# Performance work log

Measured on AMD Instinct MI355X. Metric: run time of the kernel, lower is better.

The kernel has to match this reference:

```python
import jax, jax.numpy as jnp
import numpy as np

B, C, H, W = 16, 768, 32, 32
HEADS = 12
EPS = 1e-5


def _make_rel_index(h, w):
    coords = np.stack(np.meshgrid(np.arange(h), np.arange(w), indexing='ij'))  # [2,h,w]
    cf = coords.reshape(2, -1)                      # [2,N]
    rel = cf[:, :, None] - cf[:, None, :]           # [2,N,N]
    rel = rel.transpose(1, 2, 0).copy()             # [N,N,2]
    rel[:, :, 0] += h - 1
    rel[:, :, 1] += w - 1
    rel[:, :, 0] *= 2 * w - 1
    return jnp.asarray(rel.sum(-1), dtype=jnp.int32)  # [N,N]


def setup_inputs() -> dict:
    key = jax.random.key(0)
    ks = jax.random.split(key, 8)
    s = 0.02
    return {
        'x': jax.random.normal(ks[0], (B, C, H, W), jnp.float32),
        'rpb_table': jax.random.normal(ks[1], ((2 * H - 1) * (2 * W - 1), HEADS), jnp.float32) * s,
        'g1': jnp.ones((C,), jnp.float32),
        'b1': jnp.zeros((C,), jnp.float32),
        'q_w': jax.random.normal(ks[2], (C, C), jnp.float32) * s,
        'q_b': jnp.zeros((C,), jnp.float32),
        'kv_w': jax.random.normal(ks[3], (2 * C, C), jnp.float32) * s,
        'kv_b': jnp.zeros((2 * C,), jnp.float32),
        'proj_w': jax.random.normal(ks[4], (C, C), jnp.float32) * s,
        'proj_b': jnp.zeros((C,), jnp.float32),
        'g2': jnp.ones((C,), jnp.float32),
        'b2': jnp.zeros((C,), jnp.float32),
        'fc1_w': jax.random.normal(ks[5], (4 * C, C), jnp.float32) * s,
        'fc1_b': jnp.zeros((4 * C,), jnp.float32),
        'fc2_w': jax.random.normal(ks[6], (C, 4 * C), jnp.float32) * s,
        'fc2_b': jnp.zeros((C,), jnp.float32),
        'rel_index': _make_rel_index(H, W),
    }


def _ln(t, g, b):
    m = t.mean(-1, keepdims=True)
    v = ((t - m) ** 2).mean(-1, keepdims=True)
    return (t - m) * jax.lax.rsqrt(v + EPS) * g + b


def reference(x, rpb_table, g1, b1, q_w, q_b, kv_w, kv_b, proj_w, proj_b,
              g2, b2, fc1_w, fc1_b, fc2_w, fc2_b, rel_index):
    b, c, h, w = x.shape
    n = h * w
    heads = rpb_table.shape[1]
    hd = c // heads
    scale = hd ** -0.5

    xt = x.reshape(b, c, n).transpose(0, 2, 1)  # [B,N,C]

    # --- attention branch ---
    xn = _ln(xt, g1, b1)
    q = (xn @ q_w.T + q_b).reshape(b, n, heads, hd).transpose(0, 2, 1, 3)  # [B,h,N,d]
    kv = (xn @ kv_w.T + kv_b).reshape(b, n, 2, heads, hd)
    k = kv[:, :, 0].transpose(0, 2, 1, 3)  # [B,h,N,d]
    v = kv[:, :, 1].transpose(0, 2, 1, 3)  # [B,h,N,d]
    attn = jnp.einsum('bhnd,bhmd->bhnm', q, k) * scale  # [B,h,N,N]
    bias = rpb_table[rel_index].transpose(2, 0, 1)      # [h,N,N]
    attn = jax.nn.softmax(attn + bias[None], axis=-1)
    o = jnp.einsum('bhnm,bhmd->bhnd', attn, v).transpose(0, 2, 1, 3).reshape(b, n, c)
    o = o @ proj_w.T + proj_b
    xt = xt + o

    # --- mlp branch ---
    xn = _ln(xt, g2, b2)
    h1 = jax.nn.gelu(xn @ fc1_w.T + fc1_b, approximate=False)
    xt = xt + (h1 @ fc2_w.T + fc2_b)

    return xt.transpose(0, 2, 1).reshape(b, c, h, w)
```

## Files before the change

### kernel.cpp

```cpp
#include <hip/hip_runtime.h>
#include <hip/hip_bf16.h>
#include <math.h>

typedef unsigned short u16;
typedef unsigned int u32;
typedef float f32x4 __attribute__((ext_vector_type(4)));
typedef short bf16x8 __attribute__((ext_vector_type(8)));
typedef unsigned short us4 __attribute__((ext_vector_type(4)));

struct alignas(16) F4 { float v[4]; };

static constexpr int Bb = 16;
static constexpr int Cc = 768;
static constexpr int Nn = 1024;
static constexpr int NH = 12;
static constexpr int HD = 64;
static constexpr float LOG2E = 1.4426950408889634f;

static __device__ __forceinline__ u16 f2bf(float f) {
  union { float f; unsigned u; } v; v.f = f;
  unsigned u = v.u;
  u += 0x7fffu + ((u >> 16) & 1u);
  return (u16)(u >> 16);
}
static __device__ __forceinline__ float bf2f(u16 x) {
  union { unsigned u; float f; } v; v.u = ((unsigned)x) << 16; return v.f;
}
static __device__ __forceinline__ void gload16(const u16* g, u16* l) {
  __builtin_amdgcn_global_load_lds((const __attribute__((address_space(1))) u32*)g,
                                   (__attribute__((address_space(3))) u32*)l, 16, 0, 0);
}

__global__ __launch_bounds__(256) void k_prep(const float* __restrict__ q_w,
    const float* __restrict__ kv_w, const float* __restrict__ proj_w,
    const float* __restrict__ fc1_w, const float* __restrict__ fc2_w,
    const float* __restrict__ q_b, const float* __restrict__ kv_b,
    u16* __restrict__ wqkv, u16* __restrict__ wproj, u16* __restrict__ wfc1,
    u16* __restrict__ wfc2, float* __restrict__ bqkv) {
  int i = blockIdx.x * 256 + threadIdx.x;
  if (i < 589824)            wqkv[i] = f2bf(q_w[i]);
  else if (i < 1769472)      wqkv[i] = f2bf(kv_w[i - 589824]);
  else if (i < 2359296)      wproj[i - 1769472] = f2bf(proj_w[i - 1769472]);
  else if (i < 4718592)      wfc1[i - 2359296] = f2bf(fc1_w[i - 2359296]);
  else if (i < 7077888)      wfc2[i - 4718592] = f2bf(fc2_w[i - 4718592]);
  else if (i < 7078656)      bqkv[i - 7077888] = q_b[i - 7077888];
  else                       bqkv[i - 7077888] = kv_b[i - 7078656];
}

__global__ void k_transpose(const float* __restrict__ x, float* __restrict__ xt) {
  __shared__ float tile[32][33];
  int b = blockIdx.z, c0 = blockIdx.y * 32, n0 = blockIdx.x * 32;
  int tx = threadIdx.x, ty = threadIdx.y;
  const float* xp = x + (size_t)b * Cc * Nn;
  #pragma unroll
  for (int i = 0; i < 32; i += 8)
    tile[ty + i][tx] = xp[(size_t)(c0 + ty + i) * Nn + n0 + tx];
  __syncthreads();
  float* xtp = xt + (size_t)b * Nn * Cc;
  #pragma unroll
  for (int i = 0; i < 32; i += 8)
    xtp[(size_t)(n0 + ty + i) * Cc + c0 + tx] = tile[tx][ty + i];
}

__global__ __launch_bounds__(256) void k_layernorm(const float* __restrict__ in,
    const float* __restrict__ gam, const float* __restrict__ bet,
    u16* __restrict__ out) {
  int wave = threadIdx.x >> 6, lane = threadIdx.x & 63;
  int row = blockIdx.x * 4 + wave;
  const float* p = in + (size_t)row * Cc;
  float v[12]; float s = 0.f;
  #pragma unroll
  for (int i = 0; i < 12; i++) { v[i] = p[lane + i * 64]; s += v[i]; }
  #pragma unroll
  for (int m = 32; m >= 1; m >>= 1) s += __shfl_xor(s, m);
  float mean = s * (1.f / 768.f);
  float q = 0.f;
  #pragma unroll
  for (int i = 0; i < 12; i++) { float d = v[i] - mean; q += d * d; }
  #pragma unroll
  for (int m = 32; m >= 1; m >>= 1) q += __shfl_xor(q, m);
  float rstd = rsqrtf(q * (1.f / 768.f) + 1e-5f);
  u16* o = out + (size_t)row * Cc;
  #pragma unroll
  for (int i = 0; i < 12; i++) {
    int j = lane + i * 64;
    o[j] = f2bf((v[i] - mean) * rstd * gam[j] + bet[j]);
  }
}

__global__ void k_bias_pre(const float* __restrict__ rpb, const int* __restrict__ rel,
                           u16* __restrict__ out) {
  int idx = blockIdx.x * 256 + threadIdx.x;
  int k = idx & 1023, q = (idx >> 10) & 1023, h = idx >> 20;
  float v = rpb[rel[(size_t)q * Nn + k] * NH + h];
  out[((size_t)h * Nn + q) * Nn + k] = f2bf(v * LOG2E);
}

struct GemmArgs {
  const u16* A; const u16* W; const float* bias;
  int M, N, K;
  const float* resIn;
  float* outF;
  u16* outBf;
  u16 *q, *k, *v;
};

template <int EPI>
__global__ __launch_bounds__(256) void k_gemm(GemmArgs p) {
  __shared__ __align__(16) u16 lA[128 * 32];
  __shared__ __align__(16) u16 lB[128 * 32];
  const int tid = threadIdx.x;
  const int wave = tid >> 6, lane = tid & 63;
  const int l15 = lane & 15, g = lane >> 4;
  const int wrow = wave >> 1, wcol = wave & 1;
  const int nwg = gridDim.x * gridDim.y;
  const int wg = blockIdx.y * gridDim.x + blockIdx.x;
  const int swz = (wg & 7) * (nwg >> 3) + (wg >> 3);
  const int bn = (swz % gridDim.x) * 128, bm = (swz / gridDim.x) * 128;
  const int K = p.K;
  f32x4 acc[4][4];
  #pragma unroll
  for (int i = 0; i < 4; i++)
    #pragma unroll
    for (int j = 0; j < 4; j++) acc[i][j] = (f32x4){0.f, 0.f, 0.f, 0.f};

  const u16* Ab = p.A + (size_t)bm * K;
  const u16* Wb = p.W + (size_t)bn * K;
  const int c0 = tid, c1 = tid + 256;
  const int r0 = c0 >> 2, k80 = (c0 & 3) * 8;
  const int r1 = c1 >> 2, k81 = (c1 & 3) * 8;

  for (int kt = 0; kt < K; kt += 32) {
    __syncthreads();
    gload16(Ab + (size_t)r0 * K + kt + k80, &lA[c0 * 8]);
    gload16(Ab + (size_t)r1 * K + kt + k81, &lA[c1 * 8]);
    gload16(Wb + (size_t)r0 * K + kt + k80, &lB[c0 * 8]);
    gload16(Wb + (size_t)r1 * K + kt + k81, &lB[c1 * 8]);
    __syncthreads();
    bf16x8 af[4], bfr[4];
    #pragma unroll
    for (int mt = 0; mt < 4; mt++)
      af[mt] = *(const bf16x8*)&lA[(wrow * 64 + mt * 16 + l15) * 32 + g * 8];
    #pragma unroll
    for (int nt = 0; nt < 4; nt++)
      bfr[nt] = *(const bf16x8*)&lB[(wcol * 64 + nt * 16 + l15) * 32 + g * 8];
    __builtin_amdgcn_s_setprio(1);
    #pragma unroll
    for (int mt = 0; mt < 4; mt++)
      #pragma unroll
      for (int nt = 0; nt < 4; nt++)
        acc[mt][nt] = __builtin_amdgcn_mfma_f32_16x16x32_bf16(af[mt], bfr[nt], acc[mt][nt], 0, 0, 0);
    __builtin_amdgcn_s_setprio(0);
  }

  #pragma unroll
  for (int mt = 0; mt < 4; mt++) {
    int rowb = bm + wrow * 64 + mt * 16 + g * 4;
    #pragma unroll
    for (int nt = 0; nt < 4; nt++) {
      int col = bn + wcol * 64 + nt * 16 + l15;
      float bias = p.bias[col];
      if constexpr (EPI == 0) {
        #pragma unroll
        for (int r = 0; r < 4; r++) {
          int grow = rowb + r;
          int bb = grow >> 10, nnq = grow & 1023;
          float val = acc[mt][nt][r] + bias;
          if (col < 768) {
            int head = col >> 6, d = col & 63;
            p.q[(((size_t)bb * NH + head) * Nn + nnq) * HD + d] = f2bf(val * (0.125f * LOG2E));
          } else {
            int j2 = col - 768;
            if (j2 < 768) {
              int head = j2 >> 6, d = j2 & 63;
              p.k[(((size_t)bb * NH + head) * Nn + nnq) * HD + d] = f2bf(val);
            } else {
              int j3 = j2 - 768;
              int head = j3 >> 6, d = j3 & 63;
              p.v[(((size_t)bb * NH + head) * HD + d) * Nn + nnq] = f2bf(val);
            }
          }
        }
      } else if constexpr (EPI == 1) {
        #pragma unroll
        for (int r = 0; r < 4; r++) {
          size_t idx = (size_t)(rowb + r) * p.N + col;
          p.outF[idx] = acc[mt][nt][r] + bias + p.resIn[idx];
        }
      } else if constexpr (EPI == 2) {
        #pragma unroll
        for (int r = 0; r < 4; r++) {
          float val = acc[mt][nt][r] + bias;
          val = 0.5f * val * (1.f + erff(val * 0.70710678118654752f));
          p.outBf[(size_t)(rowb + r) * p.N + col] = f2bf(val);
        }
      } else {
        int bb = rowb >> 10, n0 = rowb & 1023;
        F4 ov;
        #pragma unroll
        for (int r = 0; r < 4; r++)
          ov.v[r] = acc[mt][nt][r] + bias + p.resIn[(size_t)(rowb + r) * Cc + col];
        *(F4*)&p.outF[((size_t)bb * Cc + col) * Nn + n0] = ov;
      }
    }
  }
}

__global__ __launch_bounds__(512, 6) void k_attn(const u16* __restrict__ qt,
    const u16* __restrict__ kt_, const u16* __restrict__ vtt,
    const u16* __restrict__ bias2, u16* __restrict__ o) {
  __shared__ __align__(16) u16 lK[2][64 * 64];
  __shared__ __align__(16) u16 lV[2][64 * 64];
  __shared__ __align__(16) u16 lP[8][16 * 64];
  const int tid = threadIdx.x, wave = tid >> 6, lane = tid & 63;
  const int l15 = lane & 15, g = lane >> 4;
  const int b = blockIdx.z, h = blockIdx.y;
  const int q0 = blockIdx.x * 128 + wave * 16;
  const size_t bh  = ((size_t)b * NH + h) * Nn * HD;
  const size_t bhT = ((size_t)b * NH + h) * HD * Nn;
  const u16* biasH = bias2 + (size_t)h * Nn * Nn;
  u16* myP = &lP[wave][0];
  const float THR = 8.f * LOG2E;
  const int sRow = tid >> 3, sCol = tid & 7;
  const int h7 = l15 & 7;

  bf16x8 qa0, qa1;
  {
    const u16* qp = qt + bh + (size_t)(q0 + l15) * HD + g * 8;
    qa0 = *(const bf16x8*)qp;
    qa1 = *(const bf16x8*)(qp + 32);
  }
  f32x4 ao[4];
  float mr = -1e30f, lr = 0.f;
  #pragma unroll
  for (int d = 0; d < 4; d++) ao[d] = (f32x4){0.f, 0.f, 0.f, 0.f};

  auto issueKV = [&](int kt0, int buf) {
    int cs = (sCol ^ (sRow & 7)) << 3;
    gload16(kt_ + bh + (size_t)(kt0 + sRow) * HD + cs, &lK[buf][sRow * 64 + sCol * 8]);
    gload16(vtt + bhT + (size_t)sRow * Nn + kt0 + cs, &lV[buf][sRow * 64 + sCol * 8]);
  };

  issueKV(0, 0);
  for (int t = 0; t < 16; ++t) {
    const int kt0 = t * 64, buf = t & 1;
    asm volatile("s_waitcnt vmcnt(0) lgkmcnt(0)" ::: "memory");
    __builtin_amdgcn_s_barrier();
    __builtin_amdgcn_sched_barrier(0);
    if (t < 15) issueKV(kt0 + 64, buf ^ 1);

    us4 bvv[4];
    #pragma unroll
    for (int nt = 0; nt < 4; nt++)
      bvv[nt] = *(const us4*)(biasH + (size_t)(q0 + l15) * Nn + kt0 + nt * 16 + g * 4);

    f32x4 s[4];
    __builtin_amdgcn_s_setprio(1);
    #pragma unroll
    for (int nt = 0; nt < 4; nt++) {
      const int row = nt * 16 + l15;
      bf16x8 kb0 = *(const bf16x8*)&lK[buf][row * 64 + ((g ^ h7) << 3)];
      bf16x8 kb1 = *(const bf16x8*)&lK[buf][row * 64 + (((g + 4) ^ h7) << 3)];
      s[nt] = __builtin_amdgcn_mfma_f32_16x16x32_bf16(kb0, qa0,
                (f32x4){0.f, 0.f, 0.f, 0.f}, 0, 0, 0);
      s[nt] = __builtin_amdgcn_mfma_f32_16x16x32_bf16(kb1, qa1, s[nt], 0, 0, 0);
    }
    __builtin_amdgcn_s_setprio(0);

    #pragma unroll
    for (int nt = 0; nt < 4; nt++) {
      #pragma unroll
      for (int r = 0; r < 4; r++) s[nt][r] += bf2f(bvv[nt][r]);
    }
    float pm = fmaxf(fmaxf(s[0][0], s[0][1]), fmaxf(s[0][2], s[0][3]));
    #pragma unroll
    for (int nt = 1; nt < 4; nt++)
      pm = fmaxf(pm, fmaxf(fmaxf(s[nt][0], s[nt][1]), fmaxf(s[nt][2], s[nt][3])));
    pm = fmaxf(pm, __shfl_xor(pm, 16));
    pm = fmaxf(pm, __shfl_xor(pm, 32));
    if (__any(pm > mr + THR)) {
      float mnew = fmaxf(mr, pm);
      float fac = __builtin_amdgcn_exp2f(mr - mnew);
      lr *= fac;
      mr = mnew;
      f32x4 facO;
      #pragma unroll
      for (int r = 0; r < 4; r++) facO[r] = __shfl(fac, g * 4 + r);
      #pragma unroll
      for (int d = 0; d < 4; d++) ao[d] *= facO;
    }
    float ps = 0.f;
    #pragma unroll
    for (int nt = 0; nt < 4; nt++) {
      #pragma unroll
      for (int r = 0; r < 4; r++) {
        float pv = __builtin_amdgcn_exp2f(s[nt][r] - mr);
        s[nt][r] = pv;
        ps += pv;
      }
    }
    ps += __shfl_xor(ps, 16);
    ps += __shfl_xor(ps, 32);
    lr += ps;
    #pragma unroll
    for (int nt = 0; nt < 4; nt++) {
      u32 w0 = (u32)f2bf(s[nt][0]) | ((u32)f2bf(s[nt][1]) << 16);
      u32 w1 = (u32)f2bf(s[nt][2]) | ((u32)f2bf(s[nt][3]) << 16);
      int cbase = (((2 * nt + (g >> 1)) ^ h7) << 3) + (g & 1) * 4;
      *(u32*)&myP[l15 * 64 + cbase]     = w0;
      *(u32*)&myP[l15 * 64 + cbase + 2] = w1;
    }
    __builtin_amdgcn_s_setprio(1);
    #pragma unroll
    for (int kc = 0; kc < 2; kc++) {
      bf16x8 pa = *(const bf16x8*)&myP[l15 * 64 + (((4 * kc + g) ^ h7) << 3)];
      #pragma unroll
      for (int d = 0; d < 4; d++) {
        const int rv = d * 16 + l15;
        bf16x8 vb = *(const bf16x8*)&lV[buf][rv * 64 + (((kc * 4 + g) ^ h7) << 3)];
        ao[d] = __builtin_amdgcn_mfma_f32_16x16x32_bf16(pa, vb, ao[d], 0, 0, 0);
      }
    }
    __builtin_amdgcn_s_setprio(0);
  }
  f32x4 linv;
  #pragma unroll
  for (int r = 0; r < 4; r++) linv[r] = 1.f / __shfl(lr, g * 4 + r);
  #pragma unroll
  for (int r = 0; r < 4; r++) {
    int qg = q0 + g * 4 + r;
    u16* op = o + ((size_t)b * Nn + qg) * Cc + h * HD;
    #pragma unroll
    for (int d = 0; d < 4; d++)
      op[d * 16 + l15] = f2bf(ao[d][r] * linv[r]);
  }
}

extern "C" void kernel_launch(void* const* d_in, const int* in_sizes, int n_in,
                              void* d_out, int out_size, void* d_ws, size_t ws_size,
                              hipStream_t stream) {
  const float* x      = (const float*)d_in[0];
  const float* rpb    = (const float*)d_in[1];
  const float* g1     = (const float*)d_in[2];
  const float* b1v    = (const float*)d_in[3];
  const float* q_w    = (const float*)d_in[4];
  const float* q_b    = (const float*)d_in[5];
  const float* kv_w   = (const float*)d_in[6];
  const float* kv_b   = (const float*)d_in[7];
  const float* proj_w = (const float*)d_in[8];
  const float* proj_b = (const float*)d_in[9];
  const float* g2     = (const float*)d_in[10];
  const float* b2v    = (const float*)d_in[11];
  const float* fc1_w  = (const float*)d_in[12];
  const float* fc1_b  = (const float*)d_in[13];
  const float* fc2_w  = (const float*)d_in[14];
  const float* fc2_b  = (const float*)d_in[15];
  const int*   rel    = (const int*)d_in[16];
  float* out = (float*)d_out;

  char* ws = (char*)d_ws;
  size_t off = 0;
  auto alloc = [&](size_t bytes) -> void* {
    void* p = ws + off;
    off += (bytes + 255) & ~(size_t)255;
    return p;
  };
  u16*   wqkv  = (u16*)alloc((size_t)2304 * 768 * 2);
  u16*   wproj = (u16*)alloc((size_t)768 * 768 * 2);
  u16*   wfc1  = (u16*)alloc((size_t)3072 * 768 * 2);
  u16*   wfc2  = (u16*)alloc((size_t)768 * 3072 * 2);
  float* bqkv  = (float*)alloc((size_t)2304 * 4);
  float* xt    = (float*)alloc((size_t)16384 * 768 * 4);
  float* xt2   = (float*)alloc((size_t)16384 * 768 * 4);
  u16*   xn    = (u16*)alloc((size_t)16384 * 768 * 2);
  u16*   qb_   = (u16*)alloc((size_t)Bb * NH * Nn * HD * 2);
  u16*   kb_   = (u16*)alloc((size_t)Bb * NH * Nn * HD * 2);
  u16*   vb_   = (u16*)alloc((size_t)Bb * NH * Nn * HD * 2);
  u16*   ob_   = (u16*)alloc((size_t)16384 * 768 * 2);
  u16*   h1    = qb_;
  u16*   bias2 = (u16*)xt2;

  k_prep<<<27657, 256, 0, stream>>>(q_w, kv_w, proj_w, fc1_w, fc2_w, q_b, kv_b,
                                    wqkv, wproj, wfc1, wfc2, bqkv);

  k_transpose<<<dim3(32, 24, 16), dim3(32, 8), 0, stream>>>(x, xt);
  k_layernorm<<<4096, 256, 0, stream>>>(xt, g1, b1v, xn);
  k_bias_pre<<<49152, 256, 0, stream>>>(rpb, rel, bias2);

  GemmArgs ga = {};
  ga.A = xn; ga.W = wqkv; ga.bias = bqkv; ga.M = 16384; ga.N = 2304; ga.K = 768;
  ga.q = qb_; ga.k = kb_; ga.v = vb_;
  k_gemm<0><<<dim3(18, 128), 256, 0, stream>>>(ga);

  k_attn<<<dim3(8, NH, Bb), 512, 0, stream>>>(qb_, kb_, vb_, bias2, ob_);

  GemmArgs gp = {};
  gp.A = ob_; gp.W = wproj; gp.bias = proj_b; gp.M = 16384; gp.N = 768; gp.K = 768;
  gp.resIn = xt; gp.outF = xt2;
  k_gemm<1><<<dim3(6, 128), 256, 0, stream>>>(gp);

  k_layernorm<<<4096, 256, 0, stream>>>(xt2, g2, b2v, xn);

  GemmArgs gf1 = {};
  gf1.A = xn; gf1.W = wfc1; gf1.bias = fc1_b; gf1.M = 16384; gf1.N = 3072; gf1.K = 768;
  gf1.outBf = h1;
  k_gemm<2><<<dim3(24, 128), 256, 0, stream>>>(gf1);

  GemmArgs gf2 = {};
  gf2.A = h1; gf2.W = wfc2; gf2.bias = fc2_b; gf2.M = 16384; gf2.N = 768; gf2.K = 3072;
  gf2.resIn = xt2; gf2.outF = out;
  k_gemm<3><<<dim3(6, 128), 256, 0, stream>>>(gf2);
}
```

Before: 599.1 us.

## Rewrite GEMM as 256x256 tile double-buffered pipeline with swizzled LDS

Replaces the 128x128 single-buffered GEMM with a 256x256 tile, 512-thread kernel using K=64 steps and two dynamic-shared-memory buffers. Global loads for the next tile are interleaved between four MFMA phases, with explicit vmcnt waits and barriers. LDS columns are XOR-swizzled to avoid bank conflicts. The aim is to hide global load latency and raise arithmetic intensity per loaded byte. In exchange it needs 128KB of LDS per block, has fewer blocks in the grid (e.g. 192 for the N=768 GEMMs), and relies on hand-counted waitcnt values being correct.

```diff
diff --git a/kernel.cpp b/kernel.cpp
--- a/kernel.cpp
+++ b/kernel.cpp
@@ -9,6 +9,7 @@
 typedef unsigned short us4 __attribute__((ext_vector_type(4)));
 
 struct alignas(16) F4 { float v[4]; };
+template <int N> struct Tag { static constexpr int v = N; };
 
 static constexpr int Bb = 16;
 static constexpr int Cc = 768;
@@ -106,59 +107,126 @@
 };
 
 template <int EPI>
-__global__ __launch_bounds__(256) void k_gemm(GemmArgs p) {
-  __shared__ __align__(16) u16 lA[128 * 32];
-  __shared__ __align__(16) u16 lB[128 * 32];
+__global__ __launch_bounds__(512, 2) void k_gemm(GemmArgs p) {
+  extern __shared__ f32x4 smv[];
+  u16* lA = (u16*)smv;
+  u16* lB = (u16*)smv + 2 * 256 * 64;
   const int tid = threadIdx.x;
   const int wave = tid >> 6, lane = tid & 63;
-  const int l15 = lane & 15, g = lane >> 4;
-  const int wrow = wave >> 1, wcol = wave & 1;
+  const int l15 = lane & 15, g = lane >> 4, h7 = l15 & 7;
+  const int wr = wave >> 2, wc = wave & 3;
+  const int rl = tid >> 3, cc8 = tid & 7;
   const int nwg = gridDim.x * gridDim.y;
   const int wg = blockIdx.y * gridDim.x + blockIdx.x;
   const int swz = (wg & 7) * (nwg >> 3) + (wg >> 3);
-  const int bn = (swz % gridDim.x) * 128, bm = (swz / gridDim.x) * 128;
+  const int bn = (swz % gridDim.x) * 256, bm = (swz / gridDim.x) * 256;
   const int K = p.K;
-  f32x4 acc[4][4];
-  #pragma unroll
-  for (int i = 0; i < 4; i++)
+
+  f32x4 acc[8][4];
+  #pragma unroll
+  for (int i = 0; i < 8; i++)
     #pragma unroll
     for (int j = 0; j < 4; j++) acc[i][j] = (f32x4){0.f, 0.f, 0.f, 0.f};
 
   const u16* Ab = p.A + (size_t)bm * K;
   const u16* Wb = p.W + (size_t)bn * K;
-  const int c0 = tid, c1 = tid + 256;
-  const int r0 = c0 >> 2, k80 = (c0 & 3) * 8;
-  const int r1 = c1 >> 2, k81 = (c1 & 3) * 8;
-
-  for (int kt = 0; kt < K; kt += 32) {
-    __syncthreads();
-    gload16(Ab + (size_t)r0 * K + kt + k80, &lA[c0 * 8]);
-    gload16(Ab + (size_t)r1 * K + kt + k81, &lA[c1 * 8]);
-    gload16(Wb + (size_t)r0 * K + kt + k80, &lB[c0 * 8]);
-    gload16(Wb + (size_t)r1 * K + kt + k81, &lB[c1 * 8]);
-    __syncthreads();
-    bf16x8 af[4], bfr[4];
-    #pragma unroll
-    for (int mt = 0; mt < 4; mt++)
-      af[mt] = *(const bf16x8*)&lA[(wrow * 64 + mt * 16 + l15) * 32 + g * 8];
-    #pragma unroll
-    for (int nt = 0; nt < 4; nt++)
-      bfr[nt] = *(const bf16x8*)&lB[(wcol * 64 + nt * 16 + l15) * 32 + g * 8];
+  const int csw = (cc8 ^ (rl & 7)) * 8;
+
+  auto stageA = [&](int buf, int k0, int half) {
+    int r0 = half * 64 + rl, r1 = r0 + 128;
+    gload16(Ab + (size_t)r0 * K + k0 + csw, &lA[buf * 16384 + r0 * 64 + cc8 * 8]);
+    gload16(Ab + (size_t)r1 * K + k0 + csw, &lA[buf * 16384 + r1 * 64 + cc8 * 8]);
+  };
+  auto stageB = [&](int buf, int k0, int half) {
+    int r0 = ((rl >> 5) << 6) + half * 32 + (rl & 31), r1 = r0 + 128;
+    gload16(Wb + (size_t)r0 * K + k0 + csw, &lB[buf * 16384 + r0 * 64 + cc8 * 8]);
+    gload16(Wb + (size_t)r1 * K + k0 + csw, &lB[buf * 16384 + r1 * 64 + cc8 * 8]);
+  };
+
+  bf16x8 a[4][2], bq[4][2];
+  auto rdA = [&](int buf, int mt, int kk) {
+    int row = wr * 128 + mt * 16 + l15;
+    return *(const bf16x8*)&lA[buf * 16384 + row * 64 + (((kk << 2) + g) ^ h7) * 8];
+  };
+  auto rdB = [&](int buf, int nt, int kk) {
+    int row = wc * 64 + nt * 16 + l15;
+    return *(const bf16x8*)&lB[buf * 16384 + row * 64 + (((kk << 2) + g) ^ h7) * 8];
+  };
+  auto MF = [&](auto MBt, auto NBt) {
+    constexpr int MB = decltype(MBt)::v, NB = decltype(NBt)::v;
     __builtin_amdgcn_s_setprio(1);
     #pragma unroll
-    for (int mt = 0; mt < 4; mt++)
-      #pragma unroll
-      for (int nt = 0; nt < 4; nt++)
-        acc[mt][nt] = __builtin_amdgcn_mfma_f32_16x16x32_bf16(af[mt], bfr[nt], acc[mt][nt], 0, 0, 0);
+    for (int kk = 0; kk < 2; kk++)
+      #pragma unroll
+      for (int mi = 0; mi < 4; mi++)
+        #pragma unroll
+        for (int ni = 0; ni < 2; ni++)
+          acc[MB + mi][NB + ni] = __builtin_amdgcn_mfma_f32_16x16x32_bf16(
+              a[mi][kk], bq[NB + ni][kk], acc[MB + mi][NB + ni], 0, 0, 0);
     __builtin_amdgcn_s_setprio(0);
-  }
-
-  #pragma unroll
-  for (int mt = 0; mt < 4; mt++) {
-    int rowb = bm + wrow * 64 + mt * 16 + g * 4;
+  };
+
+  stageA(0, 0, 0); stageB(0, 0, 0); stageB(0, 0, 1); stageA(0, 0, 1);
+  stageA(1, 64, 0);
+  asm volatile("s_waitcnt vmcnt(6)" ::: "memory");
+  __builtin_amdgcn_s_barrier();
+
+  auto TILE = [&](int t, auto tag) {
+    constexpr int TAIL = decltype(tag)::v;
+    const int buf = t & 1, nb = buf ^ 1;
+    const int k1 = (t + 1) * 64;
+    #pragma unroll
+    for (int mi = 0; mi < 4; mi++) { a[mi][0] = rdA(buf, mi, 0); a[mi][1] = rdA(buf, mi, 1); }
+    #pragma unroll
+    for (int ni = 0; ni < 2; ni++) { bq[ni][0] = rdB(buf, ni, 0); bq[ni][1] = rdB(buf, ni, 1); }
+    if constexpr (TAIL < 2) {
+      stageB(nb, k1, 0);
+      asm volatile("s_waitcnt vmcnt(6)" ::: "memory");
+    } else {
+      asm volatile("s_waitcnt vmcnt(2)" ::: "memory");
+    }
+    __builtin_amdgcn_s_barrier();
+    __builtin_amdgcn_sched_barrier(0);
+    MF(Tag<0>{}, Tag<0>{});
+    #pragma unroll
+    for (int ni = 0; ni < 2; ni++) { bq[2 + ni][0] = rdB(buf, 2 + ni, 0); bq[2 + ni][1] = rdB(buf, 2 + ni, 1); }
+    if constexpr (TAIL < 2) {
+      stageB(nb, k1, 1);
+      asm volatile("s_waitcnt vmcnt(6)" ::: "memory");
+    } else {
+      asm volatile("s_waitcnt vmcnt(0)" ::: "memory");
+    }
+    __builtin_amdgcn_s_barrier();
+    __builtin_amdgcn_sched_barrier(0);
+    MF(Tag<0>{}, Tag<2>{});
+    #pragma unroll
+    for (int mi = 0; mi < 4; mi++) { a[mi][0] = rdA(buf, 4 + mi, 0); a[mi][1] = rdA(buf, 4 + mi, 1); }
+    if constexpr (TAIL < 2) stageA(nb, k1, 1);
+    __builtin_amdgcn_s_barrier();
+    __builtin_amdgcn_sched_barrier(0);
+    MF(Tag<4>{}, Tag<2>{});
+    if constexpr (TAIL == 0) {
+      stageA(buf, k1 + 64, 0);
+      asm volatile("s_waitcnt vmcnt(6)" ::: "memory");
+    } else if constexpr (TAIL == 1) {
+      asm volatile("s_waitcnt vmcnt(4)" ::: "memory");
+    }
+    __builtin_amdgcn_s_barrier();
+    __builtin_amdgcn_sched_barrier(0);
+    MF(Tag<4>{}, Tag<0>{});
+  };
+
+  const int NT = K >> 6;
+  for (int t = 0; t < NT - 2; ++t) TILE(t, Tag<0>{});
+  TILE(NT - 2, Tag<1>{});
+  TILE(NT - 1, Tag<2>{});
+
+  #pragma unroll
+  for (int mt = 0; mt < 8; mt++) {
+    int rowb = bm + wr * 128 + mt * 16 + g * 4;
     #pragma unroll
     for (int nt = 0; nt < 4; nt++) {
-      int col = bn + wcol * 64 + nt * 16 + l15;
+      int col = bn + wc * 64 + nt * 16 + l15;
       float bias = p.bias[col];
       if constexpr (EPI == 0) {
         #pragma unroll
@@ -380,6 +448,11 @@
   u16*   h1    = qb_;
   u16*   bias2 = (u16*)xt2;
 
+  hipFuncSetAttribute((const void*)k_gemm<0>, hipFuncAttributeMaxDynamicSharedMemorySize, 131072);
+  hipFuncSetAttribute((const void*)k_gemm<1>, hipFuncAttributeMaxDynamicSharedMemorySize, 131072);
+  hipFuncSetAttribute((const void*)k_gemm<2>, hipFuncAttributeMaxDynamicSharedMemorySize, 131072);
+  hipFuncSetAttribute((const void*)k_gemm<3>, hipFuncAttributeMaxDynamicSharedMemorySize, 131072);
+
   k_prep<<<27657, 256, 0, stream>>>(q_w, kv_w, proj_w, fc1_w, fc2_w, q_b, kv_b,
                                     wqkv, wproj, wfc1, wfc2, bqkv);
 
@@ -390,24 +463,24 @@
   GemmArgs ga = {};
   ga.A = xn; ga.W = wqkv; ga.bias = bqkv; ga.M = 16384; ga.N = 2304; ga.K = 768;
   ga.q = qb_; ga.k = kb_; ga.v = vb_;
-  k_gemm<0><<<dim3(18, 128), 256, 0, stream>>>(ga);
+  k_gemm<0><<<dim3(9, 64), 512, 131072, stream>>>(ga);
 
   k_attn<<<dim3(8, NH, Bb), 512, 0, stream>>>(qb_, kb_, vb_, bias2, ob_);
 
   GemmArgs gp = {};
   gp.A = ob_; gp.W = wproj; gp.bias = proj_b; gp.M = 16384; gp.N = 768; gp.K = 768;
   gp.resIn = xt; gp.outF = xt2;
-  k_gemm<1><<<dim3(6, 128), 256, 0, stream>>>(gp);
+  k_gemm<1><<<dim3(3, 64), 512, 131072, stream>>>(gp);
 
   k_layernorm<<<4096, 256, 0, stream>>>(xt2, g2, b2v, xn);
 
   GemmArgs gf1 = {};
   gf1.A = xn; gf1.W = wfc1; gf1.bias = fc1_b; gf1.M = 16384; gf1.N = 3072; gf1.K = 768;
   gf1.outBf = h1;
-  k_gemm<2><<<dim3(24, 128), 256, 0, stream>>>(gf1);
+  k_gemm<2><<<dim3(12, 64), 512, 131072, stream>>>(gf1);
 
   GemmArgs gf2 = {};
   gf2.A = h1; gf2.W = wfc2; gf2.bias = fc2_b; gf2.M = 16384; gf2.N = 768; gf2.K = 3072;
   gf2.resIn = xt2; gf2.outF = out;
-  k_gemm<3><<<dim3(6, 128), 256, 0, stream>>>(gf2);
-}
+  k_gemm<3><<<dim3(3, 64), 512, 131072, stream>>>(gf2);
+}
```

Result: faster. 574.2 us (-4.2%).
